# Performance work log

Measured on AMD Instinct MI355X. Metric: run time of the kernel, lower is better.

Reference implementation:

```python
import jax, jax.numpy as jnp
import numpy as np

N_NODES = 50000
N_EDGES = 800000
IN_C = 64
HID = 128
OUT_C = 2
N_GRAPHS = 64


def setup_inputs() -> dict:
    key = jax.random.key(0)
    ks = jax.random.split(key, 12)
    x = jax.random.normal(ks[0], (N_NODES, IN_C), dtype=jnp.float32)
    edge_index = jax.random.randint(ks[1], (2, N_EDGES), 0, N_NODES, dtype=jnp.int64)
    batch = jnp.sort(jax.random.randint(ks[2], (N_NODES,), 0, N_GRAPHS, dtype=jnp.int64))
    def glorot(k, shape):
        lim = float(np.sqrt(6.0 / (shape[0] + shape[1])))
        return jax.random.uniform(k, shape, dtype=jnp.float32, minval=-lim, maxval=lim)
    return {
        "x": x,
        "edge_index": edge_index,
        "batch": batch,
        "W1": glorot(ks[3], (IN_C, HID)),  "b1": jnp.zeros((HID,), jnp.float32),
        "W2": glorot(ks[4], (HID, HID)),   "b2": jnp.zeros((HID,), jnp.float32),
        "Wm1": glorot(ks[5], (HID, HID)),  "bm1": jnp.zeros((HID,), jnp.float32),
        "Wm2": glorot(ks[6], (HID, OUT_C)), "bm2": jnp.zeros((OUT_C,), jnp.float32),
    }


def reference(x, edge_index, batch, W1, b1, W2, b2, Wm1, bm1, Wm2, bm2):
    N = x.shape[0]
    # GCN normalization with self-loops (PyG GCNConv defaults)
    loops = jnp.arange(N, dtype=edge_index.dtype)
    src = jnp.concatenate([edge_index[0], loops])  # message sources
    dst = jnp.concatenate([edge_index[1], loops])  # aggregation targets
    deg = jax.ops.segment_sum(jnp.ones(dst.shape, x.dtype), dst, num_segments=N)
    dinv = jnp.where(deg > 0, jax.lax.rsqrt(deg), 0.0)
    norm = dinv[src] * dinv[dst]  # [E+N]

    def gcn_conv(h, W, b):
        h = h @ W                         # transform first (PyG order)
        msg = h[src] * norm[:, None]      # gather + normalize
        return jax.ops.segment_sum(msg, dst, num_segments=N) + b  # scatter-add

    h = jax.nn.relu(gcn_conv(x, W1, b1))
    # dropout is identity in eval mode
    h = gcn_conv(h, W2, b2)

    # global mean pool over graphs
    sums = jax.ops.segment_sum(h, batch, num_segments=N_GRAPHS)
    cnt = jax.ops.segment_sum(jnp.ones((N,), h.dtype), batch, num_segments=N_GRAPHS)
    g = sums / jnp.maximum(cnt, 1.0)[:, None]  # [G, HID]

    g = jax.nn.relu(g @ Wm1 + bm1)
    return g @ Wm2 + bm2  # [G, OUT_C]
```

## Files before the change

### kernel.cpp

```cpp
#include <hip/hip_runtime.h>
#include <stdint.h>

#define N_NODES 50000
#define N_EDGES 800000
#define IN_C 64
#define HID 128
#define OUT_C 2
#define N_GRAPHS 64
#define NBUCK 196
#define BCAP 6144
#define ECH 4096

typedef long long i64;
typedef __attribute__((ext_vector_type(8))) short bf8;
typedef __attribute__((ext_vector_type(4))) float f32x4;

__device__ __forceinline__ float bf2f(ushort h) {
    return __uint_as_float(((uint)h) << 16);
}
__device__ __forceinline__ ushort f2bf(float f) {
    uint x = __float_as_uint(f);
    uint r = x + 0x7fffu + ((x >> 16) & 1u);
    return (ushort)(r >> 16);
}
__device__ __forceinline__ float loadf(const void* p, size_t i, int bf) {
    return bf ? bf2f(((const ushort*)p)[i]) : ((const float*)p)[i];
}
__device__ __forceinline__ int clampi(int v, int lo, int hi) {
    return min(max(v, lo), hi);
}

__device__ __forceinline__ int edge_src(const void* ei, int e, int wide) {
    return wide ? (int)((const i64*)ei)[e] : ((const int*)ei)[e];
}
__device__ __forceinline__ int edge_dst(const void* ei, int e, int wide) {
    return wide ? (int)((const i64*)ei)[N_EDGES + e] : ((const int*)ei)[N_EDGES + e];
}
__device__ __forceinline__ i64 batch_at(const void* b, int i, int wide) {
    return wide ? ((const i64*)b)[i] : (i64)((const int*)b)[i];
}

__device__ __forceinline__ void bacc(float* a, uint4 u) {
    a[0] += bf2f((ushort)(u.x & 0xffffu)); a[1] += bf2f((ushort)(u.x >> 16));
    a[2] += bf2f((ushort)(u.y & 0xffffu)); a[3] += bf2f((ushort)(u.y >> 16));
    a[4] += bf2f((ushort)(u.z & 0xffffu)); a[5] += bf2f((ushort)(u.z >> 16));
    a[6] += bf2f((ushort)(u.w & 0xffffu)); a[7] += bf2f((ushort)(u.w >> 16));
}
__device__ __forceinline__ uint pk2(float lo, float hi) {
    return ((uint)f2bf(hi) << 16) | (uint)f2bf(lo);
}
__device__ __forceinline__ uint4 bpack(const float* a, float dv) {
    uint4 o;
    o.x = pk2(a[0] * dv, a[1] * dv);
    o.y = pk2(a[2] * dv, a[3] * dv);
    o.z = pk2(a[4] * dv, a[5] * dv);
    o.w = pk2(a[6] * dv, a[7] * dv);
    return o;
}

__global__ __launch_bounds__(256) void k_init(const uint* __restrict__ braw,
                                              const uint* __restrict__ xraw,
                                              int* __restrict__ bcnt,
                                              float* __restrict__ gbuf,
                                              int* __restrict__ iflag,
                                              int* __restrict__ fflag) {
    int i = blockIdx.x * blockDim.x + threadIdx.x;
    if (i < N_GRAPHS * HID) gbuf[i] = 0.f;
    if (i < NBUCK) bcnt[i] = 0;
    if (blockIdx.x == 0) {
        __shared__ uint si[128];
        __shared__ int sf[256];
        int t = threadIdx.x;
        if (t < 128) si[t] = (t < 100) ? braw[25001 + 2 * t] : 0u;
        uint e = (xraw[t] >> 7) & 0xFFu;
        sf[t] = (e >= 100u && e <= 140u) ? 1 : 0;
        __syncthreads();
        for (int off = 128; off > 0; off >>= 1) {
            if (t < off) {
                sf[t] += sf[t + off];
                if (off <= 64 && t < 64) si[t] |= si[t + off];
            }
            __syncthreads();
        }
        if (t == 0) {
            *iflag = (si[0] == 0u) ? 1 : 0;
            *fflag = (sf[0] >= 192) ? 1 : 0;
        }
    }
}

__global__ __launch_bounds__(1024) void k_binA(const void* __restrict__ ei,
                                               const int* __restrict__ iflag,
                                               const int* __restrict__ fflag,
                                               const void* __restrict__ W1,
                                               const void* __restrict__ W2,
                                               ushort* __restrict__ Wt1,
                                               ushort* __restrict__ Wt2,
                                               int* __restrict__ bcnt,
                                               uint2* __restrict__ bmem) {
    int t = threadIdx.x;
    if (t < 256 && blockIdx.x < (IN_C * HID + HID * HID) / 256) {
        int ff = *fflag;
        int idx = blockIdx.x * 256 + t;
        if (idx < IN_C * HID) {
            int k = idx >> 7, n = idx & 127;
            Wt1[n * IN_C + k] = f2bf(loadf(W1, idx, ff));
        } else {
            int j = idx - IN_C * HID;
            int k = j >> 7, n = j & 127;
            Wt2[n * HID + k] = f2bf(loadf(W2, j, ff));
        }
    }
    int wide = *iflag;
    __shared__ int cnt[NBUCK];
    __shared__ int obase[NBUCK];
    __shared__ int run[NBUCK];
    __shared__ int gbase[NBUCK];
    __shared__ int sc[256];
    __shared__ uint2 stage[ECH];
    int e0 = blockIdx.x * ECH;
    int m = min(ECH, N_EDGES - e0);
    for (int i = t; i < NBUCK; i += 1024) cnt[i] = 0;
    __syncthreads();
    for (int i = t; i < m; i += 1024) {
        int d = edge_dst(ei, e0 + i, wide);
        atomicAdd(&cnt[d >> 8], 1);
    }
    __syncthreads();
    int cv = (t < NBUCK) ? cnt[t] : 0;
    if (t < 256) sc[t] = cv;
    __syncthreads();
    for (int off = 1; off < 256; off <<= 1) {
        int v = (t >= off && t < 256) ? sc[t - off] : 0;
        __syncthreads();
        if (t < 256) sc[t] += v;
        __syncthreads();
    }
    if (t < NBUCK) {
        int ex = sc[t] - cv;
        obase[t] = ex;
        run[t] = ex;
        gbase[t] = (cv > 0) ? atomicAdd(&bcnt[t], cv) : 0;
    }
    __syncthreads();
    for (int i = t; i < m; i += 1024) {
        int s = edge_src(ei, e0 + i, wide);
        int d = edge_dst(ei, e0 + i, wide);
        int slot = atomicAdd(&run[d >> 8], 1);
        uint2 pr; pr.x = (uint)s; pr.y = (uint)d;
        stage[slot] = pr;
    }
    __syncthreads();
    for (int i = t; i < m; i += 1024) {
        uint2 pr = stage[i];
        int b = (int)(pr.y >> 8);
        int pos = gbase[b] + (i - obase[b]);
        if (pos < BCAP) bmem[(size_t)b * BCAP + pos] = pr;
    }
}

__global__ __launch_bounds__(1024) void k_binB(const uint2* __restrict__ bmem,
                                               const int* __restrict__ bcnt,
                                               const void* __restrict__ x,
                                               const int* __restrict__ fflag,
                                               int* __restrict__ offs,
                                               int* __restrict__ csr,
                                               float* __restrict__ dinv,
                                               ushort* __restrict__ Y1) {
    int b = blockIdx.x;
    int t = threadIdx.x;
    int node0 = b << 8;
    __shared__ int sc[256];
    __shared__ int degl[256];
    __shared__ int run[256];
    __shared__ float sdinv[256];
    __shared__ int sbase, scnt;
    __shared__ int stage[BCAP];
    int v = (t < NBUCK) ? bcnt[t] : 0;
    if (t < 256) sc[t] = v;
    __syncthreads();
    for (int off = 1; off < 256; off <<= 1) {
        int u = (t >= off && t < 256) ? sc[t - off] : 0;
        __syncthreads();
        if (t < 256) sc[t] += u;
        __syncthreads();
    }
    if (t == b) {
        int c = clampi(v, 0, BCAP);
        scnt = c;
        sbase = clampi(sc[t] - v, 0, N_EDGES - c);
    }
    if (t < 256) degl[t] = 0;
    __syncthreads();
    int cnt = scnt;
    int base = sbase;
    for (int i = t; i < cnt; i += 1024) {
        uint2 pr = bmem[(size_t)b * BCAP + i];
        atomicAdd(&degl[pr.y & 255], 1);
    }
    __syncthreads();
    int dv = (t < 256) ? degl[t] : 0;
    if (t < 256) sc[t] = dv;
    __syncthreads();
    for (int off = 1; off < 256; off <<= 1) {
        int u = (t >= off && t < 256) ? sc[t - off] : 0;
        __syncthreads();
        if (t < 256) sc[t] += u;
        __syncthreads();
    }
    if (t < 256) {
        int ex = sc[t] - dv;
        run[t] = ex;
        float di = rsqrtf((float)(dv + 1));
        sdinv[t] = di;
        int n = node0 + t;
        if (n < N_NODES) { offs[n] = base + ex; dinv[n] = di; }
    }
    if (b == 0 && t == 0) offs[N_NODES] = N_EDGES;
    __syncthreads();
    for (int i = t; i < cnt; i += 1024) {
        uint2 pr = bmem[(size_t)b * BCAP + i];
        int slot = atomicAdd(&run[pr.y & 255], 1);
        stage[clampi(slot, 0, BCAP - 1)] = (int)pr.x;
    }
    __syncthreads();
    for (int i = t; i < cnt; i += 1024) csr[base + i] = stage[i];
    int ff = *fflag;
    for (int idx = t; idx < 256 * (IN_C / 4); idx += 1024) {
        int nl = idx >> 4, c4 = (idx & 15) * 4;
        int nn = node0 + nl;
        if (nn < N_NODES) {
            float x0, x1, x2, x3;
            if (ff) {
                ushort4 u = *(const ushort4*)((const ushort*)x + (size_t)nn * IN_C + c4);
                x0 = bf2f(u.x); x1 = bf2f(u.y); x2 = bf2f(u.z); x3 = bf2f(u.w);
            } else {
                float4 vv = *(const float4*)((const float*)x + (size_t)nn * IN_C + c4);
                x0 = vv.x; x1 = vv.y; x2 = vv.z; x3 = vv.w;
            }
            float di = sdinv[nl];
            ushort4 o;
            o.x = f2bf(x0 * di); o.y = f2bf(x1 * di);
            o.z = f2bf(x2 * di); o.w = f2bf(x3 * di);
            *(ushort4*)(Y1 + (size_t)nn * IN_C + c4) = o;
        }
    }
}

__global__ __launch_bounds__(256) void k_aggM(const ushort* __restrict__ Y1,
                                              const float* __restrict__ dinv,
                                              const int* __restrict__ offs,
                                              const int* __restrict__ csr,
                                              ushort* __restrict__ M) {
    int n = (blockIdx.x * blockDim.x + threadIdx.x) >> 3;
    int lane = threadIdx.x & 7;
    if (n >= N_NODES) return;
    const uint4* y4 = (const uint4*)Y1;
    size_t rb = (size_t)n * 8 + lane;
    float a[8];
    {
        uint4 su = y4[rb];
        a[0] = bf2f((ushort)(su.x & 0xffffu)); a[1] = bf2f((ushort)(su.x >> 16));
        a[2] = bf2f((ushort)(su.y & 0xffffu)); a[3] = bf2f((ushort)(su.y >> 16));
        a[4] = bf2f((ushort)(su.z & 0xffffu)); a[5] = bf2f((ushort)(su.z >> 16));
        a[6] = bf2f((ushort)(su.w & 0xffffu)); a[7] = bf2f((ushort)(su.w >> 16));
    }
    int s = offs[n];
    int e = min(offs[n + 1], s + 4096);
    int i = s;
    for (; i + 8 <= e; i += 8) {
        uint4 u[8];
#pragma unroll
        for (int k = 0; k < 8; k++)
            u[k] = y4[(size_t)csr[i + k] * 8 + lane];
#pragma unroll
        for (int k = 0; k < 8; k++) bacc(a, u[k]);
    }
    for (; i < e; i++) bacc(a, y4[(size_t)csr[i] * 8 + lane]);
    ((uint4*)M)[rb] = bpack(a, dinv[n]);
}

__global__ __launch_bounds__(256) void k_agg128(const ushort* __restrict__ hs,
                                                const float* __restrict__ dinv,
                                                const int* __restrict__ offs,
                                                const int* __restrict__ csr,
                                                ushort* __restrict__ out) {
    int n = (blockIdx.x * blockDim.x + threadIdx.x) >> 4;
    int lane = threadIdx.x & 15;
    if (n >= N_NODES) return;
    const uint4* h4 = (const uint4*)hs;
    size_t rb = (size_t)n * 16 + lane;
    float a[8];
    {
        uint4 su = h4[rb];
        a[0] = bf2f((ushort)(su.x & 0xffffu)); a[1] = bf2f((ushort)(su.x >> 16));
        a[2] = bf2f((ushort)(su.y & 0xffffu)); a[3] = bf2f((ushort)(su.y >> 16));
        a[4] = bf2f((ushort)(su.z & 0xffffu)); a[5] = bf2f((ushort)(su.z >> 16));
        a[6] = bf2f((ushort)(su.w & 0xffffu)); a[7] = bf2f((ushort)(su.w >> 16));
    }
    int s = offs[n];
    int e = min(offs[n + 1], s + 4096);
    int i = s;
    for (; i + 8 <= e; i += 8) {
        uint4 u[8];
#pragma unroll
        for (int k = 0; k < 8; k++)
            u[k] = h4[(size_t)csr[i + k] * 16 + lane];
#pragma unroll
        for (int k = 0; k < 8; k++) bacc(a, u[k]);
    }
    for (; i < e; i++) bacc(a, h4[(size_t)csr[i] * 16 + lane]);
    ((uint4*)out)[rb] = bpack(a, dinv[n]);
}

template <int K>
__global__ __launch_bounds__(256) void k_gemm_f(const ushort* __restrict__ A,
                                                const ushort* __restrict__ Wt,
                                                const int* __restrict__ fflag,
                                                const float* __restrict__ dinv,
                                                const void* __restrict__ bias,
                                                ushort* __restrict__ out) {
    int ff = *fflag;
    int wave = threadIdx.x >> 6;
    int lane = threadIdx.x & 63;
    int m16 = lane & 15;
    int q = lane >> 4;
    int rowbase = blockIdx.x * 64 + wave * 16;
    int arow = min(rowbase + m16, N_NODES - 1);

    f32x4 acc[8];
#pragma unroll
    for (int t = 0; t < 8; t++) acc[t] = (f32x4){0.f, 0.f, 0.f, 0.f};
#pragma unroll
    for (int kc = 0; kc < K; kc += 32) {
        bf8 a = *(const bf8*)(A + (size_t)arow * K + kc + q * 8);
#pragma unroll
        for (int t = 0; t < 8; t++) {
            bf8 b = *(const bf8*)(Wt + (size_t)(t * 16 + m16) * K + kc + q * 8);
            acc[t] = __builtin_amdgcn_mfma_f32_16x16x32_bf16(a, b, acc[t], 0, 0, 0);
        }
    }
    float dv[4];
    int rowok[4];
#pragma unroll
    for (int r = 0; r < 4; r++) {
        int row = rowbase + q * 4 + r;
        rowok[r] = (row < N_NODES);
        dv[r] = rowok[r] ? dinv[row] : 1.f;
    }
#pragma unroll
    for (int t = 0; t < 8; t++) {
        int col = t * 16 + m16;
        float bv = loadf(bias, col, ff);
#pragma unroll
        for (int r = 0; r < 4; r++) {
            int row = rowbase + q * 4 + r;
            if (rowok[r]) {
                float v = fmaxf(acc[t][r] + bv, 0.f) * dv[r];
                out[(size_t)row * HID + col] = f2bf(v);
            }
        }
    }
}

__global__ __launch_bounds__(256) void k_gemm_pool(const ushort* __restrict__ A,
                                                   const ushort* __restrict__ Wt,
                                                   const void* __restrict__ batch,
                                                   const int* __restrict__ iflag,
                                                   float* __restrict__ gsum) {
    const int K = HID;
    int wide = *iflag;
    int tid = threadIdx.x;
    int wave = tid >> 6;
    int lane = tid & 63;
    int m16 = lane & 15;
    int q = lane >> 4;
    int rowbase = blockIdx.x * 64 + wave * 16;
    int arow = min(rowbase + m16, N_NODES - 1);

    __shared__ float sacc[64][HID];
    __shared__ int sbg[64];

    if (tid < 64) {
        int n = blockIdx.x * 64 + tid;
        int g = (n < N_NODES) ? (int)batch_at(batch, n, wide) : -1;
        sbg[tid] = (g < 0 || g >= N_GRAPHS) ? -1 : g;
    }
    f32x4 acc[8];
#pragma unroll
    for (int t = 0; t < 8; t++) acc[t] = (f32x4){0.f, 0.f, 0.f, 0.f};
#pragma unroll
    for (int kc = 0; kc < K; kc += 32) {
        bf8 a = *(const bf8*)(A + (size_t)arow * K + kc + q * 8);
#pragma unroll
        for (int t = 0; t < 8; t++) {
            bf8 b = *(const bf8*)(Wt + (size_t)(t * 16 + m16) * K + kc + q * 8);
            acc[t] = __builtin_amdgcn_mfma_f32_16x16x32_bf16(a, b, acc[t], 0, 0, 0);
        }
    }
#pragma unroll
    for (int t = 0; t < 8; t++) {
        int col = t * 16 + m16;
#pragma unroll
        for (int r = 0; r < 4; r++) {
            int rl = wave * 16 + q * 4 + r;
            int row = rowbase + q * 4 + r;
            sacc[rl][col] = (row < N_NODES) ? acc[t][r] : 0.f;
        }
    }
    __syncthreads();
    int col = tid & 127;
    int half = tid >> 7;
    int gcur = -1;
    float a = 0.f;
    for (int r = half * 32; r < half * 32 + 32; r++) {
        int g = sbg[r];
        if (g != gcur) {
            if (gcur >= 0) atomicAdd(&gsum[gcur * HID + col], a);
            a = 0.f;
            gcur = g;
        }
        a += sacc[r][col];
    }
    if (gcur >= 0) atomicAdd(&gsum[gcur * HID + col], a);
}

__global__ void k_mlp(const float* __restrict__ gsum, const void* __restrict__ batch,
                      const int* __restrict__ iflag, const void* __restrict__ b2,
                      const void* __restrict__ Wm1, const void* __restrict__ bm1,
                      const void* __restrict__ Wm2, const void* __restrict__ bm2,
                      const int* __restrict__ fflag, float* __restrict__ out) {
    int ff = *fflag;
    int wide = *iflag;
    int gr = blockIdx.x;
    int c = threadIdx.x;
    int lo = 0, hi = N_NODES;
    while (lo < hi) { int m = (lo + hi) >> 1; if (batch_at(batch, m, wide) < (i64)gr) lo = m + 1; else hi = m; }
    int s = lo;
    lo = s; hi = N_NODES;
    while (lo < hi) { int m = (lo + hi) >> 1; if (batch_at(batch, m, wide) < (i64)(gr + 1)) lo = m + 1; else hi = m; }
    float cnt = (float)(lo - s);

    __shared__ float sg[HID];
    __shared__ float r0[HID], r1[HID];
    sg[c] = gsum[gr * HID + c] / fmaxf(cnt, 1.0f) + loadf(b2, c, ff);
    __syncthreads();
    float acc = loadf(bm1, c, ff);
#pragma unroll 8
    for (int k = 0; k < HID; k++) acc += sg[k] * loadf(Wm1, k * HID + c, ff);
    float hid = fmaxf(acc, 0.f);
    r0[c] = hid * loadf(Wm2, c * OUT_C + 0, ff);
    r1[c] = hid * loadf(Wm2, c * OUT_C + 1, ff);
    __syncthreads();
    for (int off = 64; off > 0; off >>= 1) {
        if (c < off) { r0[c] += r0[c + off]; r1[c] += r1[c + off]; }
        __syncthreads();
    }
    if (c == 0) {
        out[gr * OUT_C + 0] = r0[0] + loadf(bm2, 0, ff);
        out[gr * OUT_C + 1] = r1[0] + loadf(bm2, 1, ff);
    }
}


extern "C" void kernel_launch(void* const* d_in, const int* in_sizes, int n_in,
                              void* d_out, int out_size, void* d_ws, size_t ws_size,
                              hipStream_t stream) {
    const void* x     = d_in[0];
    const void* ei    = d_in[1];
    const void* batch = d_in[2];
    const void* W1  = d_in[3];
    const void* b1  = d_in[4];
    const void* W2  = d_in[5];
    const void* b2  = d_in[6];
    const void* Wm1 = d_in[7];
    const void* bm1 = d_in[8];
    const void* Wm2 = d_in[9];
    const void* bm2 = d_in[10];

    char* p = (char*)d_ws;
    auto alloc = [&](size_t bytes) {
        char* r = p;
        p += (bytes + 255) & ~(size_t)255;
        return r;
    };
    int*    iflag  = (int*)alloc(4);
    int*    fflag  = (int*)alloc(4);
    int*    bcnt   = (int*)alloc(NBUCK * 4);
    uint2*  bmem   = (uint2*)alloc((size_t)NBUCK * BCAP * 8);
    float*  dinv   = (float*)alloc(N_NODES * 4);
    int*    offs   = (int*)alloc((N_NODES + 1) * 4);
    int*    csr    = (int*)alloc(N_EDGES * 4);
    ushort* Wt1    = (ushort*)alloc(IN_C * HID * 2);
    ushort* Wt2    = (ushort*)alloc(HID * HID * 2);
    ushort* Y1     = (ushort*)alloc((size_t)N_NODES * IN_C * 2);
    ushort* Mbuf   = (ushort*)alloc((size_t)N_NODES * IN_C * 2);
    ushort* h1s    = (ushort*)alloc((size_t)N_NODES * HID * 2);
    ushort* N2     = (ushort*)alloc((size_t)N_NODES * HID * 2);
    float*  gbuf   = (float*)alloc(N_GRAPHS * HID * 4);

    k_init<<<(N_GRAPHS * HID + 255) / 256, 256, 0, stream>>>(
        (const uint*)batch, (const uint*)x, bcnt, gbuf, iflag, fflag);
    k_binA<<<(N_EDGES + ECH - 1) / ECH, 1024, 0, stream>>>(
        ei, iflag, fflag, W1, W2, Wt1, Wt2, bcnt, bmem);
    k_binB<<<NBUCK, 1024, 0, stream>>>(bmem, bcnt, x, fflag, offs, csr, dinv, Y1);

    k_aggM<<<(N_NODES * 8 + 255) / 256, 256, 0, stream>>>(Y1, dinv, offs, csr, Mbuf);
    k_gemm_f<IN_C><<<(N_NODES + 63) / 64, 256, 0, stream>>>(Mbuf, Wt1, fflag, dinv, b1, h1s);
    k_agg128<<<(N_NODES * 16 + 255) / 256, 256, 0, stream>>>(h1s, dinv, offs, csr, N2);
    k_gemm_pool<<<(N_NODES + 63) / 64, 256, 0, stream>>>(N2, Wt2, batch, iflag, gbuf);

    k_mlp<<<N_GRAPHS, HID, 0, stream>>>(gbuf, batch, iflag, b2, Wm1, bm1, Wm2, bm2, fflag, (float*)d_out);
}
```

Before: 206.3 us.

## Fuse neighbor aggregation into MFMA GEMM kernels for both GCN layers

```diff
diff --git a/kernel.cpp b/kernel.cpp
--- a/kernel.cpp
+++ b/kernel.cpp
@@ -40,6 +40,12 @@
     return wide ? ((const i64*)b)[i] : (i64)((const int*)b)[i];
 }
 
+__device__ __forceinline__ void bset(float* a, uint4 u) {
+    a[0] = bf2f((ushort)(u.x & 0xffffu)); a[1] = bf2f((ushort)(u.x >> 16));
+    a[2] = bf2f((ushort)(u.y & 0xffffu)); a[3] = bf2f((ushort)(u.y >> 16));
+    a[4] = bf2f((ushort)(u.z & 0xffffu)); a[5] = bf2f((ushort)(u.z >> 16));
+    a[6] = bf2f((ushort)(u.w & 0xffffu)); a[7] = bf2f((ushort)(u.w >> 16));
+}
 __device__ __forceinline__ void bacc(float* a, uint4 u) {
     a[0] += bf2f((ushort)(u.x & 0xffffu)); a[1] += bf2f((ushort)(u.x >> 16));
     a[2] += bf2f((ushort)(u.y & 0xffffu)); a[3] += bf2f((ushort)(u.y >> 16));
@@ -49,13 +55,13 @@
 __device__ __forceinline__ uint pk2(float lo, float hi) {
     return ((uint)f2bf(hi) << 16) | (uint)f2bf(lo);
 }
-__device__ __forceinline__ uint4 bpack(const float* a, float dv) {
-    uint4 o;
-    o.x = pk2(a[0] * dv, a[1] * dv);
-    o.y = pk2(a[2] * dv, a[3] * dv);
-    o.z = pk2(a[4] * dv, a[5] * dv);
-    o.w = pk2(a[6] * dv, a[7] * dv);
-    return o;
+__device__ __forceinline__ bf8 packbf8(const float* a, float dv) {
+    union { bf8 v; uint u[4]; } r;
+    r.u[0] = pk2(a[0] * dv, a[1] * dv);
+    r.u[1] = pk2(a[2] * dv, a[3] * dv);
+    r.u[2] = pk2(a[4] * dv, a[5] * dv);
+    r.u[3] = pk2(a[6] * dv, a[7] * dv);
+    return r.v;
 }
 
 __global__ __launch_bounds__(256) void k_init(const uint* __restrict__ braw,
@@ -247,98 +253,59 @@
     }
 }
 
-__global__ __launch_bounds__(256) void k_aggM(const ushort* __restrict__ Y1,
-                                              const float* __restrict__ dinv,
-                                              const int* __restrict__ offs,
-                                              const int* __restrict__ csr,
-                                              ushort* __restrict__ M) {
-    int n = (blockIdx.x * blockDim.x + threadIdx.x) >> 3;
-    int lane = threadIdx.x & 7;
-    if (n >= N_NODES) return;
-    const uint4* y4 = (const uint4*)Y1;
-    size_t rb = (size_t)n * 8 + lane;
-    float a[8];
-    {
-        uint4 su = y4[rb];
-        a[0] = bf2f((ushort)(su.x & 0xffffu)); a[1] = bf2f((ushort)(su.x >> 16));
-        a[2] = bf2f((ushort)(su.y & 0xffffu)); a[3] = bf2f((ushort)(su.y >> 16));
-        a[4] = bf2f((ushort)(su.z & 0xffffu)); a[5] = bf2f((ushort)(su.z >> 16));
-        a[6] = bf2f((ushort)(su.w & 0xffffu)); a[7] = bf2f((ushort)(su.w >> 16));
-    }
-    int s = offs[n];
-    int e = min(offs[n + 1], s + 4096);
-    int i = s;
-    for (; i + 8 <= e; i += 8) {
-        uint4 u[8];
-#pragma unroll
-        for (int k = 0; k < 8; k++)
-            u[k] = y4[(size_t)csr[i + k] * 8 + lane];
-#pragma unroll
-        for (int k = 0; k < 8; k++) bacc(a, u[k]);
-    }
-    for (; i < e; i++) bacc(a, y4[(size_t)csr[i] * 8 + lane]);
-    ((uint4*)M)[rb] = bpack(a, dinv[n]);
-}
-
-__global__ __launch_bounds__(256) void k_agg128(const ushort* __restrict__ hs,
-                                                const float* __restrict__ dinv,
-                                                const int* __restrict__ offs,
-                                                const int* __restrict__ csr,
-                                                ushort* __restrict__ out) {
-    int n = (blockIdx.x * blockDim.x + threadIdx.x) >> 4;
-    int lane = threadIdx.x & 15;
-    if (n >= N_NODES) return;
-    const uint4* h4 = (const uint4*)hs;
-    size_t rb = (size_t)n * 16 + lane;
-    float a[8];
-    {
-        uint4 su = h4[rb];
-        a[0] = bf2f((ushort)(su.x & 0xffffu)); a[1] = bf2f((ushort)(su.x >> 16));
-        a[2] = bf2f((ushort)(su.y & 0xffffu)); a[3] = bf2f((ushort)(su.y >> 16));
-        a[4] = bf2f((ushort)(su.z & 0xffffu)); a[5] = bf2f((ushort)(su.z >> 16));
-        a[6] = bf2f((ushort)(su.w & 0xffffu)); a[7] = bf2f((ushort)(su.w >> 16));
-    }
-    int s = offs[n];
-    int e = min(offs[n + 1], s + 4096);
-    int i = s;
-    for (; i + 8 <= e; i += 8) {
-        uint4 u[8];
-#pragma unroll
-        for (int k = 0; k < 8; k++)
-            u[k] = h4[(size_t)csr[i + k] * 16 + lane];
-#pragma unroll
-        for (int k = 0; k < 8; k++) bacc(a, u[k]);
-    }
-    for (; i < e; i++) bacc(a, h4[(size_t)csr[i] * 16 + lane]);
-    ((uint4*)out)[rb] = bpack(a, dinv[n]);
-}
-
-template <int K>
-__global__ __launch_bounds__(256) void k_gemm_f(const ushort* __restrict__ A,
-                                                const ushort* __restrict__ Wt,
-                                                const int* __restrict__ fflag,
-                                                const float* __restrict__ dinv,
-                                                const void* __restrict__ bias,
-                                                ushort* __restrict__ out) {
+__global__ __launch_bounds__(256) void k_l1(const ushort* __restrict__ Y1,
+                                            const float* __restrict__ dinv,
+                                            const int* __restrict__ offs,
+                                            const int* __restrict__ csr,
+                                            const ushort* __restrict__ Wt,
+                                            const int* __restrict__ fflag,
+                                            const void* __restrict__ bias,
+                                            ushort* __restrict__ out) {
     int ff = *fflag;
     int wave = threadIdx.x >> 6;
     int lane = threadIdx.x & 63;
     int m16 = lane & 15;
     int q = lane >> 4;
     int rowbase = blockIdx.x * 64 + wave * 16;
-    int arow = min(rowbase + m16, N_NODES - 1);
+    int n = min(rowbase + m16, N_NODES - 1);
+
+    const uint4* y4 = (const uint4*)Y1;
+    size_t rb = (size_t)n * 8 + q;
+    float a0[8], a1[8];
+    bset(a0, y4[rb]);
+    bset(a1, y4[rb + 4]);
+    int s = offs[n];
+    int e = min(offs[n + 1], s + 4096);
+    int i = s;
+    for (; i + 4 <= e; i += 4) {
+        uint4 u[4][2];
+#pragma unroll
+        for (int k = 0; k < 4; k++) {
+            size_t r = (size_t)csr[i + k] * 8 + q;
+            u[k][0] = y4[r];
+            u[k][1] = y4[r + 4];
+        }
+#pragma unroll
+        for (int k = 0; k < 4; k++) { bacc(a0, u[k][0]); bacc(a1, u[k][1]); }
+    }
+    for (; i < e; i++) {
+        size_t r = (size_t)csr[i] * 8 + q;
+        bacc(a0, y4[r]);
+        bacc(a1, y4[r + 4]);
+    }
+    float dvn = dinv[n];
+    bf8 af0 = packbf8(a0, dvn);
+    bf8 af1 = packbf8(a1, dvn);
 
     f32x4 acc[8];
 #pragma unroll
     for (int t = 0; t < 8; t++) acc[t] = (f32x4){0.f, 0.f, 0.f, 0.f};
 #pragma unroll
-    for (int kc = 0; kc < K; kc += 32) {
-        bf8 a = *(const bf8*)(A + (size_t)arow * K + kc + q * 8);
-#pragma unroll
-        for (int t = 0; t < 8; t++) {
-            bf8 b = *(const bf8*)(Wt + (size_t)(t * 16 + m16) * K + kc + q * 8);
-            acc[t] = __builtin_amdgcn_mfma_f32_16x16x32_bf16(a, b, acc[t], 0, 0, 0);
-        }
+    for (int t = 0; t < 8; t++) {
+        bf8 b0 = *(const bf8*)(Wt + (size_t)(t * 16 + m16) * IN_C + q * 8);
+        acc[t] = __builtin_amdgcn_mfma_f32_16x16x32_bf16(af0, b0, acc[t], 0, 0, 0);
+        bf8 b1 = *(const bf8*)(Wt + (size_t)(t * 16 + m16) * IN_C + 32 + q * 8);
+        acc[t] = __builtin_amdgcn_mfma_f32_16x16x32_bf16(af1, b1, acc[t], 0, 0, 0);
     }
     float dv[4];
     int rowok[4];
@@ -363,12 +330,14 @@
     }
 }
 
-__global__ __launch_bounds__(256) void k_gemm_pool(const ushort* __restrict__ A,
-                                                   const ushort* __restrict__ Wt,
-                                                   const void* __restrict__ batch,
-                                                   const int* __restrict__ iflag,
-                                                   float* __restrict__ gsum) {
-    const int K = HID;
+__global__ __launch_bounds__(256) void k_l2(const ushort* __restrict__ hs,
+                                            const float* __restrict__ dinv,
+                                            const int* __restrict__ offs,
+                                            const int* __restrict__ csr,
+                                            const ushort* __restrict__ Wt,
+                                            const void* __restrict__ batch,
+                                            const int* __restrict__ iflag,
+                                            float* __restrict__ gsum) {
     int wide = *iflag;
     int tid = threadIdx.x;
     int wave = tid >> 6;
@@ -376,27 +345,65 @@
     int m16 = lane & 15;
     int q = lane >> 4;
     int rowbase = blockIdx.x * 64 + wave * 16;
-    int arow = min(rowbase + m16, N_NODES - 1);
+    int n = min(rowbase + m16, N_NODES - 1);
 
     __shared__ float sacc[64][HID];
     __shared__ int sbg[64];
-
     if (tid < 64) {
-        int n = blockIdx.x * 64 + tid;
-        int g = (n < N_NODES) ? (int)batch_at(batch, n, wide) : -1;
+        int nn = blockIdx.x * 64 + tid;
+        int g = (nn < N_NODES) ? (int)batch_at(batch, nn, wide) : -1;
         sbg[tid] = (g < 0 || g >= N_GRAPHS) ? -1 : g;
     }
+
+    const uint4* h4 = (const uint4*)hs;
+    size_t rb = (size_t)n * 16 + q;
+    float a[4][8];
+    bset(a[0], h4[rb]);
+    bset(a[1], h4[rb + 4]);
+    bset(a[2], h4[rb + 8]);
+    bset(a[3], h4[rb + 12]);
+    int s = offs[n];
+    int e = min(offs[n + 1], s + 4096);
+    int i = s;
+    for (; i + 2 <= e; i += 2) {
+        uint4 u[2][4];
+#pragma unroll
+        for (int kk = 0; kk < 2; kk++) {
+            size_t r = (size_t)csr[i + kk] * 16 + q;
+            u[kk][0] = h4[r];
+            u[kk][1] = h4[r + 4];
+            u[kk][2] = h4[r + 8];
+            u[kk][3] = h4[r + 12];
+        }
+#pragma unroll
+        for (int kk = 0; kk < 2; kk++) {
+#pragma unroll
+            for (int k = 0; k < 4; k++) bacc(a[k], u[kk][k]);
+        }
+    }
+    for (; i < e; i++) {
+        size_t r = (size_t)csr[i] * 16 + q;
+        bacc(a[0], h4[r]);
+        bacc(a[1], h4[r + 4]);
+        bacc(a[2], h4[r + 8]);
+        bacc(a[3], h4[r + 12]);
+    }
+    float dvn = dinv[n];
+    bf8 af0 = packbf8(a[0], dvn);
+    bf8 af1 = packbf8(a[1], dvn);
+    bf8 af2 = packbf8(a[2], dvn);
+    bf8 af3 = packbf8(a[3], dvn);
+
     f32x4 acc[8];
 #pragma unroll
     for (int t = 0; t < 8; t++) acc[t] = (f32x4){0.f, 0.f, 0.f, 0.f};
 #pragma unroll
-    for (int kc = 0; kc < K; kc += 32) {
-        bf8 a = *(const bf8*)(A + (size_t)arow * K + kc + q * 8);
-#pragma unroll
-        for (int t = 0; t < 8; t++) {
-            bf8 b = *(const bf8*)(Wt + (size_t)(t * 16 + m16) * K + kc + q * 8);
-            acc[t] = __builtin_amdgcn_mfma_f32_16x16x32_bf16(a, b, acc[t], 0, 0, 0);
-        }
+    for (int t = 0; t < 8; t++) {
+        const ushort* wr = Wt + (size_t)(t * 16 + m16) * HID + q * 8;
+        acc[t] = __builtin_amdgcn_mfma_f32_16x16x32_bf16(af0, *(const bf8*)(wr), acc[t], 0, 0, 0);
+        acc[t] = __builtin_amdgcn_mfma_f32_16x16x32_bf16(af1, *(const bf8*)(wr + 32), acc[t], 0, 0, 0);
+        acc[t] = __builtin_amdgcn_mfma_f32_16x16x32_bf16(af2, *(const bf8*)(wr + 64), acc[t], 0, 0, 0);
+        acc[t] = __builtin_amdgcn_mfma_f32_16x16x32_bf16(af3, *(const bf8*)(wr + 96), acc[t], 0, 0, 0);
     }
 #pragma unroll
     for (int t = 0; t < 8; t++) {
@@ -412,17 +419,17 @@
     int col = tid & 127;
     int half = tid >> 7;
     int gcur = -1;
-    float a = 0.f;
+    float av = 0.f;
     for (int r = half * 32; r < half * 32 + 32; r++) {
         int g = sbg[r];
         if (g != gcur) {
-            if (gcur >= 0) atomicAdd(&gsum[gcur * HID + col], a);
-            a = 0.f;
+            if (gcur >= 0) atomicAdd(&gsum[gcur * HID + col], av);
+            av = 0.f;
             gcur = g;
         }
-        a += sacc[r][col];
-    }
-    if (gcur >= 0) atomicAdd(&gsum[gcur * HID + col], a);
+        av += sacc[r][col];
+    }
+    if (gcur >= 0) atomicAdd(&gsum[gcur * HID + col], av);
 }
 
 __global__ void k_mlp(const float* __restrict__ gsum, const void* __restrict__ batch,
@@ -494,9 +501,7 @@
     ushort* Wt1    = (ushort*)alloc(IN_C * HID * 2);
     ushort* Wt2    = (ushort*)alloc(HID * HID * 2);
     ushort* Y1     = (ushort*)alloc((size_t)N_NODES * IN_C * 2);
-    ushort* Mbuf   = (ushort*)alloc((size_t)N_NODES * IN_C * 2);
     ushort* h1s    = (ushort*)alloc((size_t)N_NODES * HID * 2);
-    ushort* N2     = (ushort*)alloc((size_t)N_NODES * HID * 2);
     float*  gbuf   = (float*)alloc(N_GRAPHS * HID * 4);
 
     k_init<<<(N_GRAPHS * HID + 255) / 256, 256, 0, stream>>>(
@@ -505,10 +510,8 @@
         ei, iflag, fflag, W1, W2, Wt1, Wt2, bcnt, bmem);
     k_binB<<<NBUCK, 1024, 0, stream>>>(bmem, bcnt, x, fflag, offs, csr, dinv, Y1);
 
-    k_aggM<<<(N_NODES * 8 + 255) / 256, 256, 0, stream>>>(Y1, dinv, offs, csr, Mbuf);
-    k_gemm_f<IN_C><<<(N_NODES + 63) / 64, 256, 0, stream>>>(Mbuf, Wt1, fflag, dinv, b1, h1s);
-    k_agg128<<<(N_NODES * 16 + 255) / 256, 256, 0, stream>>>(h1s, dinv, offs, csr, N2);
-    k_gemm_pool<<<(N_NODES + 63) / 64, 256, 0, stream>>>(N2, Wt2, batch, iflag, gbuf);
+    k_l1<<<(N_NODES + 63) / 64, 256, 0, stream>>>(Y1, dinv, offs, csr, Wt1, fflag, b1, h1s);
+    k_l2<<<(N_NODES + 63) / 64, 256, 0, stream>>>(h1s, dinv, offs, csr, Wt2, batch, iflag, gbuf);
 
     k_mlp<<<N_GRAPHS, HID, 0, stream>>>(gbuf, batch, iflag, b2, Wm1, bm1, Wm2, bm2, fflag, (float*)d_out);
 }
```

After: 209.7 us. No clear change (+1.7%).

## Split node feature buffers into 32-channel column slabs for cache-friendly gathers

Applied to the files above, without the earlier changes.

```diff
diff --git a/kernel.cpp b/kernel.cpp
--- a/kernel.cpp
+++ b/kernel.cpp
@@ -40,22 +40,12 @@
     return wide ? ((const i64*)b)[i] : (i64)((const int*)b)[i];
 }
 
-__device__ __forceinline__ void bacc(float* a, uint4 u) {
+__device__ __forceinline__ void bacc4(float* a, uint2 u) {
     a[0] += bf2f((ushort)(u.x & 0xffffu)); a[1] += bf2f((ushort)(u.x >> 16));
     a[2] += bf2f((ushort)(u.y & 0xffffu)); a[3] += bf2f((ushort)(u.y >> 16));
-    a[4] += bf2f((ushort)(u.z & 0xffffu)); a[5] += bf2f((ushort)(u.z >> 16));
-    a[6] += bf2f((ushort)(u.w & 0xffffu)); a[7] += bf2f((ushort)(u.w >> 16));
 }
 __device__ __forceinline__ uint pk2(float lo, float hi) {
     return ((uint)f2bf(hi) << 16) | (uint)f2bf(lo);
-}
-__device__ __forceinline__ uint4 bpack(const float* a, float dv) {
-    uint4 o;
-    o.x = pk2(a[0] * dv, a[1] * dv);
-    o.y = pk2(a[2] * dv, a[3] * dv);
-    o.z = pk2(a[4] * dv, a[5] * dv);
-    o.w = pk2(a[6] * dv, a[7] * dv);
-    return o;
 }
 
 __global__ __launch_bounds__(256) void k_init(const uint* __restrict__ braw,
@@ -242,75 +232,48 @@
             ushort4 o;
             o.x = f2bf(x0 * di); o.y = f2bf(x1 * di);
             o.z = f2bf(x2 * di); o.w = f2bf(x3 * di);
-            *(ushort4*)(Y1 + (size_t)nn * IN_C + c4) = o;
-        }
-    }
-}
-
-__global__ __launch_bounds__(256) void k_aggM(const ushort* __restrict__ Y1,
+            int g = c4 >> 5;
+            *(ushort4*)(Y1 + ((size_t)g * N_NODES + nn) * 32 + (c4 & 31)) = o;
+        }
+    }
+}
+
+template <int SHIFT>
+__global__ __launch_bounds__(256) void k_aggS(const ushort* __restrict__ src,
                                               const float* __restrict__ dinv,
                                               const int* __restrict__ offs,
                                               const int* __restrict__ csr,
-                                              ushort* __restrict__ M) {
-    int n = (blockIdx.x * blockDim.x + threadIdx.x) >> 3;
+                                              ushort* __restrict__ out) {
+    int g = blockIdx.x & ((1 << SHIFT) - 1);
+    int chunk = blockIdx.x >> SHIFT;
+    int n = (chunk * 256 + (int)threadIdx.x) >> 3;
     int lane = threadIdx.x & 7;
     if (n >= N_NODES) return;
-    const uint4* y4 = (const uint4*)Y1;
+    const uint2* s2 = (const uint2*)(src + (size_t)g * N_NODES * 32);
     size_t rb = (size_t)n * 8 + lane;
-    float a[8];
+    float a[4];
     {
-        uint4 su = y4[rb];
+        uint2 su = s2[rb];
         a[0] = bf2f((ushort)(su.x & 0xffffu)); a[1] = bf2f((ushort)(su.x >> 16));
         a[2] = bf2f((ushort)(su.y & 0xffffu)); a[3] = bf2f((ushort)(su.y >> 16));
-        a[4] = bf2f((ushort)(su.z & 0xffffu)); a[5] = bf2f((ushort)(su.z >> 16));
-        a[6] = bf2f((ushort)(su.w & 0xffffu)); a[7] = bf2f((ushort)(su.w >> 16));
     }
     int s = offs[n];
     int e = min(offs[n + 1], s + 4096);
     int i = s;
     for (; i + 8 <= e; i += 8) {
-        uint4 u[8];
+        uint2 u[8];
 #pragma unroll
         for (int k = 0; k < 8; k++)
-            u[k] = y4[(size_t)csr[i + k] * 8 + lane];
-#pragma unroll
-        for (int k = 0; k < 8; k++) bacc(a, u[k]);
-    }
-    for (; i < e; i++) bacc(a, y4[(size_t)csr[i] * 8 + lane]);
-    ((uint4*)M)[rb] = bpack(a, dinv[n]);
-}
-
-__global__ __launch_bounds__(256) void k_agg128(const ushort* __restrict__ hs,
-                                                const float* __restrict__ dinv,
-                                                const int* __restrict__ offs,
-                                                const int* __restrict__ csr,
-                                                ushort* __restrict__ out) {
-    int n = (blockIdx.x * blockDim.x + threadIdx.x) >> 4;
-    int lane = threadIdx.x & 15;
-    if (n >= N_NODES) return;
-    const uint4* h4 = (const uint4*)hs;
-    size_t rb = (size_t)n * 16 + lane;
-    float a[8];
-    {
-        uint4 su = h4[rb];
-        a[0] = bf2f((ushort)(su.x & 0xffffu)); a[1] = bf2f((ushort)(su.x >> 16));
-        a[2] = bf2f((ushort)(su.y & 0xffffu)); a[3] = bf2f((ushort)(su.y >> 16));
-        a[4] = bf2f((ushort)(su.z & 0xffffu)); a[5] = bf2f((ushort)(su.z >> 16));
-        a[6] = bf2f((ushort)(su.w & 0xffffu)); a[7] = bf2f((ushort)(su.w >> 16));
-    }
-    int s = offs[n];
-    int e = min(offs[n + 1], s + 4096);
-    int i = s;
-    for (; i + 8 <= e; i += 8) {
-        uint4 u[8];
-#pragma unroll
-        for (int k = 0; k < 8; k++)
-            u[k] = h4[(size_t)csr[i + k] * 16 + lane];
-#pragma unroll
-        for (int k = 0; k < 8; k++) bacc(a, u[k]);
-    }
-    for (; i < e; i++) bacc(a, h4[(size_t)csr[i] * 16 + lane]);
-    ((uint4*)out)[rb] = bpack(a, dinv[n]);
+            u[k] = s2[(size_t)csr[i + k] * 8 + lane];
+#pragma unroll
+        for (int k = 0; k < 8; k++) bacc4(a, u[k]);
+    }
+    for (; i < e; i++) bacc4(a, s2[(size_t)csr[i] * 8 + lane]);
+    float dv = dinv[n];
+    uint2 o;
+    o.x = pk2(a[0] * dv, a[1] * dv);
+    o.y = pk2(a[2] * dv, a[3] * dv);
+    ((uint2*)(out + (size_t)g * N_NODES * 32))[rb] = o;
 }
 
 template <int K>
@@ -333,7 +296,7 @@
     for (int t = 0; t < 8; t++) acc[t] = (f32x4){0.f, 0.f, 0.f, 0.f};
 #pragma unroll
     for (int kc = 0; kc < K; kc += 32) {
-        bf8 a = *(const bf8*)(A + (size_t)arow * K + kc + q * 8);
+        bf8 a = *(const bf8*)(A + ((size_t)(kc >> 5) * N_NODES + arow) * 32 + q * 8);
 #pragma unroll
         for (int t = 0; t < 8; t++) {
             bf8 b = *(const bf8*)(Wt + (size_t)(t * 16 + m16) * K + kc + q * 8);
@@ -352,12 +315,13 @@
     for (int t = 0; t < 8; t++) {
         int col = t * 16 + m16;
         float bv = loadf(bias, col, ff);
+        ushort* og = out + (size_t)(col >> 5) * N_NODES * 32 + (col & 31);
 #pragma unroll
         for (int r = 0; r < 4; r++) {
             int row = rowbase + q * 4 + r;
             if (rowok[r]) {
                 float v = fmaxf(acc[t][r] + bv, 0.f) * dv[r];
-                out[(size_t)row * HID + col] = f2bf(v);
+                og[(size_t)row * 32] = f2bf(v);
             }
         }
     }
@@ -391,7 +355,7 @@
     for (int t = 0; t < 8; t++) acc[t] = (f32x4){0.f, 0.f, 0.f, 0.f};
 #pragma unroll
     for (int kc = 0; kc < K; kc += 32) {
-        bf8 a = *(const bf8*)(A + (size_t)arow * K + kc + q * 8);
+        bf8 a = *(const bf8*)(A + ((size_t)(kc >> 5) * N_NODES + arow) * 32 + q * 8);
 #pragma unroll
         for (int t = 0; t < 8; t++) {
             bf8 b = *(const bf8*)(Wt + (size_t)(t * 16 + m16) * K + kc + q * 8);
@@ -493,22 +457,23 @@
     int*    csr    = (int*)alloc(N_EDGES * 4);
     ushort* Wt1    = (ushort*)alloc(IN_C * HID * 2);
     ushort* Wt2    = (ushort*)alloc(HID * HID * 2);
-    ushort* Y1     = (ushort*)alloc((size_t)N_NODES * IN_C * 2);
-    ushort* Mbuf   = (ushort*)alloc((size_t)N_NODES * IN_C * 2);
-    ushort* h1s    = (ushort*)alloc((size_t)N_NODES * HID * 2);
-    ushort* N2     = (ushort*)alloc((size_t)N_NODES * HID * 2);
+    ushort* Y1g    = (ushort*)alloc((size_t)N_NODES * IN_C * 2);
+    ushort* Mg     = (ushort*)alloc((size_t)N_NODES * IN_C * 2);
+    ushort* h1g    = (ushort*)alloc((size_t)N_NODES * HID * 2);
+    ushort* N2g    = (ushort*)alloc((size_t)N_NODES * HID * 2);
     float*  gbuf   = (float*)alloc(N_GRAPHS * HID * 4);
 
     k_init<<<(N_GRAPHS * HID + 255) / 256, 256, 0, stream>>>(
         (const uint*)batch, (const uint*)x, bcnt, gbuf, iflag, fflag);
     k_binA<<<(N_EDGES + ECH - 1) / ECH, 1024, 0, stream>>>(
         ei, iflag, fflag, W1, W2, Wt1, Wt2, bcnt, bmem);
-    k_binB<<<NBUCK, 1024, 0, stream>>>(bmem, bcnt, x, fflag, offs, csr, dinv, Y1);
-
-    k_aggM<<<(N_NODES * 8 + 255) / 256, 256, 0, stream>>>(Y1, dinv, offs, csr, Mbuf);
-    k_gemm_f<IN_C><<<(N_NODES + 63) / 64, 256, 0, stream>>>(Mbuf, Wt1, fflag, dinv, b1, h1s);
-    k_agg128<<<(N_NODES * 16 + 255) / 256, 256, 0, stream>>>(h1s, dinv, offs, csr, N2);
-    k_gemm_pool<<<(N_NODES + 63) / 64, 256, 0, stream>>>(N2, Wt2, batch, iflag, gbuf);
+    k_binB<<<NBUCK, 1024, 0, stream>>>(bmem, bcnt, x, fflag, offs, csr, dinv, Y1g);
+
+    int cpg = (N_NODES * 8 + 255) / 256;
+    k_aggS<1><<<cpg * 2, 256, 0, stream>>>(Y1g, dinv, offs, csr, Mg);
+    k_gemm_f<IN_C><<<(N_NODES + 63) / 64, 256, 0, stream>>>(Mg, Wt1, fflag, dinv, b1, h1g);
+    k_aggS<2><<<cpg * 4, 256, 0, stream>>>(h1g, dinv, offs, csr, N2g);
+    k_gemm_pool<<<(N_NODES + 63) / 64, 256, 0, stream>>>(N2g, Wt2, batch, iflag, gbuf);
 
     k_mlp<<<N_GRAPHS, HID, 0, stream>>>(gbuf, batch, iflag, b2, Wm1, bm1, Wm2, bm2, fflag, (float*)d_out);
 }
```

Measured after the change: 204.4 us. About the same (-0.9%).
